# Kernel optimization log

Hardware: AMD Instinct MI355X
Metric: run time of the kernel (lower is better)

Reference implementation:

```python
import jax, jax.numpy as jnp
import numpy as np

N_NODES = 50000
N_EDGES = 1600000
IN_DIM = 128
HID = 128
N_GRAPHS = 64
N_CLASSES = 1


def _seg_sum(x, ids, n):
    return jax.ops.segment_sum(x, ids, num_segments=n)


def _gcn_layer(h, W, b, src, dst, src_isqrt, dst_isqrt):
    # DGL GraphConv, norm='both': D_dst^{-1/2} A D_src^{-1/2} (h W) + b
    hw = h @ W                                  # [N, out]
    msg = (hw * src_isqrt[:, None])[src]        # gather -> [E, out]
    agg = _seg_sum(msg, dst, h.shape[0])        # scatter-add -> [N, out]
    return agg * dst_isqrt[:, None] + b


def setup_inputs() -> dict:
    key = jax.random.key(0)
    ks = jax.random.split(key, 16)
    x = jax.random.normal(ks[0], (N_NODES, IN_DIM), dtype=jnp.float32)
    src = jax.random.randint(ks[1], (N_EDGES,), 0, N_NODES)
    dst = jax.random.randint(ks[2], (N_EDGES,), 0, N_NODES)
    graph_id = jnp.sort(jax.random.randint(ks[3], (N_NODES,), 0, N_GRAPHS))
    s = 1.0 / np.sqrt(HID)
    params = {
        'W1': jax.random.uniform(ks[4], (IN_DIM, HID), jnp.float32, -s, s),
        'b1': jnp.zeros((HID,), jnp.float32),
        'W2': jax.random.uniform(ks[5], (HID, HID), jnp.float32, -s, s),
        'b2': jnp.zeros((HID,), jnp.float32),
        'Wc1': jax.random.uniform(ks[6], (HID, HID // 2), jnp.float32, -s, s),
        'bc1': jnp.zeros((HID // 2,), jnp.float32),
        'Wc2': jax.random.uniform(ks[7], (HID // 2, HID // 4), jnp.float32, -s, s),
        'bc2': jnp.zeros((HID // 4,), jnp.float32),
        'Wc3': jax.random.uniform(ks[8], (HID // 4, HID // 8), jnp.float32, -s, s),
        'bc3': jnp.zeros((HID // 8,), jnp.float32),
        'Wc4': jax.random.uniform(ks[9], (HID // 8, N_CLASSES), jnp.float32, -s, s),
        'bc4': jnp.zeros((N_CLASSES,), jnp.float32),
    }
    return dict(x=x, src=src, dst=dst, graph_id=graph_id, num_graphs=N_GRAPHS, **params)


def reference(x, src, dst, graph_id, num_graphs, W1, b1, W2, b2,
              Wc1, bc1, Wc2, bc2, Wc3, bc3, Wc4, bc4):
    n = x.shape[0]
    ones = jnp.ones((src.shape[0],), x.dtype)
    out_deg = jnp.clip(_seg_sum(ones, src, n), 1.0)
    in_deg = jnp.clip(_seg_sum(ones, dst, n), 1.0)
    src_isqrt = jax.lax.rsqrt(out_deg)
    dst_isqrt = jax.lax.rsqrt(in_deg)

    h = jax.nn.relu(_gcn_layer(x, W1, b1, src, dst, src_isqrt, dst_isqrt))
    h = jax.nn.relu(_gcn_layer(h, W2, b2, src, dst, src_isqrt, dst_isqrt))

    # dgl.mean_nodes: per-graph mean of node features
    sums = _seg_sum(h, graph_id, num_graphs)                       # [G, HID]
    cnts = jnp.clip(_seg_sum(jnp.ones((n,), h.dtype), graph_id, num_graphs), 1.0)
    hg = sums / cnts[:, None]

    o = jax.nn.relu(hg @ Wc1 + bc1)
    o = jax.nn.relu(o @ Wc2 + bc2)
    o = jax.nn.relu(o @ Wc3 + bc3)
    return o @ Wc4 + bc4
```

## Files before the change

### kernel.cpp

```cpp
#include <hip/hip_runtime.h>
#include <hip/hip_fp16.h>

#define FDIM 128
#define NGRAPH 64
#define POOL_CHUNK 64
#define CBLK 256
#define OCHUNK 12800
#define OBLK 64

typedef _Float16 f16;
typedef f16 f16x8 __attribute__((ext_vector_type(8)));
typedef float f32x4 __attribute__((ext_vector_type(4)));
typedef float f32x2 __attribute__((ext_vector_type(2)));

__device__ __forceinline__ int lower_bound_i(const int* a, int n, int v) {
    int lo = 0, hi = n;
    while (lo < hi) { int m = (lo + hi) >> 1; if (a[m] < v) lo = m + 1; else hi = m; }
    return lo;
}

__global__ __launch_bounds__(256) void k_pre(
        const float* __restrict__ W1, f16* __restrict__ W1h, f16* __restrict__ W1l,
        const float* __restrict__ W2, f16* __restrict__ W2h, f16* __restrict__ W2l,
        float* __restrict__ hg, const int* __restrict__ dst, int* __restrict__ partial,
        int E, int NBIN, int CE4) {
    __shared__ int lds[4 * 257];
    const int t = threadIdx.x;
    int b = blockIdx.x;
    if (b < 128) {
        int i = b * 256 + t;
        if (i < NGRAPH * FDIM) hg[i] = 0.f;
        int j = i & 16383;
        int k = j >> 7, n = j & 127;
        const float* W = (i < 16384) ? W1 : W2;
        f16* Wh = (i < 16384) ? W1h : W2h;
        f16* Wl = (i < 16384) ? W1l : W2l;
        float v = W[j];
        f16 hi = (f16)v;
        Wh[n * FDIM + k] = hi;
        Wl[n * FDIM + k] = (f16)(v - (float)hi);
    } else {
        b -= 128;
        for (int i = t; i < 4 * 257; i += 256) lds[i] = 0;
        __syncthreads();
        const int wv = t >> 6;
        int* hh = &lds[wv * 257];
        const int s = b * CE4, e = min(E, s + CE4);
        for (int i = s + t * 4; i < e; i += 1024) {
            if (i + 4 <= e) {
                uint4 d4 = *(const uint4*)&dst[i];
                atomicAdd(&hh[d4.x >> 8], 1);
                atomicAdd(&hh[d4.y >> 8], 1);
                atomicAdd(&hh[d4.z >> 8], 1);
                atomicAdd(&hh[d4.w >> 8], 1);
            } else {
                for (int j = i; j < e; j++) atomicAdd(&hh[dst[j] >> 8], 1);
            }
        }
        __syncthreads();
        for (int i = t; i < NBIN; i += 256)
            partial[i * CBLK + b] = lds[i] + lds[257 + i] + lds[514 + i] + lds[771 + i];
    }
}

__global__ __launch_bounds__(256) void k_scan_oh(
        const int* __restrict__ partial, int* __restrict__ offs, int* __restrict__ bsum,
        int M, const int* __restrict__ src, int* __restrict__ out_part,
        int E, int N, int NBIN) {
    __shared__ int lds[OCHUNK];
    const int t = threadIdx.x;
    int b = blockIdx.x;
    if (b < NBIN) {
        int i = b * 256 + t;
        int v = (i < M) ? partial[i] : 0;
        lds[t] = v;
        __syncthreads();
        for (int off = 1; off < 256; off <<= 1) {
            int x = (t >= off) ? lds[t - off] : 0;
            __syncthreads();
            lds[t] += x;
            __syncthreads();
        }
        if (i < M) offs[i] = lds[t] - v;
        if (t == 255) bsum[b] = lds[t];
    } else {
        b -= NBIN;
        const int c = b / OBLK, sl = b % OBLK;
        for (int i = t; i < OCHUNK; i += 256) lds[i] = 0;
        __syncthreads();
        const int lo = c * OCHUNK;
        const int SE = (E + OBLK - 1) / OBLK;
        const int s = sl * SE, e = min(E, s + SE);
        for (int i = s + t * 4; i < e; i += 1024) {
            if (i + 4 <= e) {
                uint4 s4 = *(const uint4*)&src[i];
                int v0 = (int)s4.x - lo, v1 = (int)s4.y - lo;
                int v2 = (int)s4.z - lo, v3 = (int)s4.w - lo;
                if ((unsigned)v0 < (unsigned)OCHUNK) atomicAdd(&lds[v0], 1);
                if ((unsigned)v1 < (unsigned)OCHUNK) atomicAdd(&lds[v1], 1);
                if ((unsigned)v2 < (unsigned)OCHUNK) atomicAdd(&lds[v2], 1);
                if ((unsigned)v3 < (unsigned)OCHUNK) atomicAdd(&lds[v3], 1);
            } else {
                for (int j = i; j < e; j++) {
                    int v = src[j] - lo;
                    if ((unsigned)v < (unsigned)OCHUNK) atomicAdd(&lds[v], 1);
                }
            }
        }
        __syncthreads();
        const int hi = min(N - lo, OCHUNK);
        for (int i = t; i < hi; i += 256)
            out_part[(size_t)sl * N + lo + i] = lds[i];
    }
}

__global__ __launch_bounds__(256) void k_coarse_scatter(
        const int* __restrict__ src, const int* __restrict__ dst,
        const int* __restrict__ offs, const int* __restrict__ bsum,
        unsigned* __restrict__ coarse_buf, int E, int CE4, int NBIN) {
    __shared__ int cur[256], sb[256];
    const int t = threadIdx.x, b = blockIdx.x;
    int v = (t < NBIN) ? bsum[t] : 0;
    sb[t] = v;
    __syncthreads();
    for (int off = 1; off < 256; off <<= 1) {
        int x = (t >= off) ? sb[t - off] : 0;
        __syncthreads();
        sb[t] += x;
        __syncthreads();
    }
    if (t < NBIN) cur[t] = offs[t * CBLK + b] + (sb[t] - v);
    __syncthreads();
    const int s = b * CE4, e = min(E, s + CE4);
    for (int i = s + t * 4; i < e; i += 1024) {
        if (i + 4 <= e) {
            uint4 d4 = *(const uint4*)&dst[i];
            uint4 s4 = *(const uint4*)&src[i];
            int p0 = atomicAdd(&cur[d4.x >> 8], 1);
            int p1 = atomicAdd(&cur[d4.y >> 8], 1);
            int p2 = atomicAdd(&cur[d4.z >> 8], 1);
            int p3 = atomicAdd(&cur[d4.w >> 8], 1);
            coarse_buf[p0] = (d4.x << 16) | s4.x;
            coarse_buf[p1] = (d4.y << 16) | s4.y;
            coarse_buf[p2] = (d4.z << 16) | s4.z;
            coarse_buf[p3] = (d4.w << 16) | s4.w;
        } else {
            for (int j = i; j < e; j++) {
                unsigned d = (unsigned)dst[j];
                int p = atomicAdd(&cur[d >> 8], 1);
                coarse_buf[p] = (d << 16) | (unsigned)src[j];
            }
        }
    }
}

template<bool IN_F16>
__device__ __forceinline__ void gemm_body(
        f16* smem, float* sisql, int blk,
        const void* __restrict__ Xv, const f16* __restrict__ Wh,
        const f16* __restrict__ Wl, const int* __restrict__ out_part,
        float* __restrict__ sisq, unsigned char* __restrict__ out, int N) {
    const int t = threadIdx.x;
    const int w = t >> 6;
    const int lane = t & 63;
    const int base = blk * 128;

    if (t < 128) {
        int row = base + t;
        float sv = 1.f;
        if (row < N) {
            if (IN_F16) {
                sv = sisq[row];
            } else {
                int a = 0;
#pragma unroll
                for (int bb = 0; bb < OBLK; bb++) a += out_part[(size_t)bb * N + row];
                sv = rsqrtf((float)max(a, 1));
                sisq[row] = sv;
            }
        }
        sisql[t] = sv;
    }
    for (int i = t; i < 2048; i += 256) {
        int n = i >> 4, kc = (i & 15) * 8;
        *(uint4*)&smem[n * 136 + kc] = *(const uint4*)&Wh[n * FDIM + kc];
    }
    __syncthreads();

    const int mrow = lane & 15;
    const int kq = (lane >> 4) * 8;
    const int arow0 = min(base + w * 32 + mrow, N - 1);
    const int arow1 = min(base + w * 32 + 16 + mrow, N - 1);

    f16x8 a0[4], a1[4];
    if (IN_F16) {
        const f16* X = (const f16*)Xv;
#pragma unroll
        for (int kk = 0; kk < 4; kk++) {
            a0[kk] = *(const f16x8*)&X[(size_t)arow0 * FDIM + kk * 32 + kq];
            a1[kk] = *(const f16x8*)&X[(size_t)arow1 * FDIM + kk * 32 + kq];
        }
    } else {
        const float* X = (const float*)Xv;
#pragma unroll
        for (int kk = 0; kk < 4; kk++) {
            float4 u0 = *(const float4*)&X[(size_t)arow0 * FDIM + kk * 32 + kq];
            float4 u1 = *(const float4*)&X[(size_t)arow0 * FDIM + kk * 32 + kq + 4];
            float4 v0 = *(const float4*)&X[(size_t)arow1 * FDIM + kk * 32 + kq];
            float4 v1 = *(const float4*)&X[(size_t)arow1 * FDIM + kk * 32 + kq + 4];
            f16x8 av;
            av[0] = (f16)u0.x; av[1] = (f16)u0.y; av[2] = (f16)u0.z; av[3] = (f16)u0.w;
            av[4] = (f16)u1.x; av[5] = (f16)u1.y; av[6] = (f16)u1.z; av[7] = (f16)u1.w;
            a0[kk] = av;
            av[0] = (f16)v0.x; av[1] = (f16)v0.y; av[2] = (f16)v0.z; av[3] = (f16)v0.w;
            av[4] = (f16)v1.x; av[5] = (f16)v1.y; av[6] = (f16)v1.z; av[7] = (f16)v1.w;
            a1[kk] = av;
        }
    }

    f32x4 acc0[8], acc1[8];
#pragma unroll
    for (int nt = 0; nt < 8; nt++) {
        acc0[nt] = (f32x4){0.f, 0.f, 0.f, 0.f};
        acc1[nt] = (f32x4){0.f, 0.f, 0.f, 0.f};
    }

#pragma unroll
    for (int kk = 0; kk < 4; kk++) {
#pragma unroll
        for (int nt = 0; nt < 8; nt++) {
            f16x8 bh = *(const f16x8*)&smem[(nt * 16 + mrow) * 136 + kk * 32 + kq];
            f16x8 bl = *(const f16x8*)&Wl[(nt * 16 + mrow) * FDIM + kk * 32 + kq];
            acc0[nt] = __builtin_amdgcn_mfma_f32_16x16x32_f16(a0[kk], bh, acc0[nt], 0, 0, 0);
            acc1[nt] = __builtin_amdgcn_mfma_f32_16x16x32_f16(a1[kk], bh, acc1[nt], 0, 0, 0);
            acc0[nt] = __builtin_amdgcn_mfma_f32_16x16x32_f16(a0[kk], bl, acc0[nt], 0, 0, 0);
            acc1[nt] = __builtin_amdgcn_mfma_f32_16x16x32_f16(a1[kk], bl, acc1[nt], 0, 0, 0);
        }
    }

    const int r0 = (lane >> 4) * 4;
    float sv0[4], sv1[4];
#pragma unroll
    for (int j = 0; j < 4; j++) {
        sv0[j] = sisql[w * 32 + r0 + j];
        sv1[j] = sisql[w * 32 + 16 + r0 + j];
    }
    __syncthreads();
#pragma unroll
    for (int nt = 0; nt < 8; nt++) {
        int c = nt * 16 + mrow;
#pragma unroll
        for (int j = 0; j < 4; j++) {
            smem[(w * 32 + r0 + j) * 136 + c]      = (f16)(acc0[nt][j] * sv0[j]);
            smem[(w * 32 + 16 + r0 + j) * 136 + c] = (f16)(acc1[nt][j] * sv1[j]);
        }
    }
    __syncthreads();
    {
        int r = t >> 1, cb = (t & 1) * 64;
        int row = base + r;
        if (row < N) {
            unsigned char* dstp = out + (size_t)row * FDIM + cb;
#pragma unroll
            for (int g2 = 0; g2 < 4; g2++) {
                unsigned wv[4];
#pragma unroll
                for (int k2 = 0; k2 < 4; k2++) {
                    const f16* p = &smem[r * 136 + cb + g2 * 16 + k2 * 4];
                    int w0 = __builtin_amdgcn_cvt_pk_fp8_f32((float)p[0], (float)p[1], 0, false);
                    w0 = __builtin_amdgcn_cvt_pk_fp8_f32((float)p[2], (float)p[3], w0, true);
                    wv[k2] = (unsigned)w0;
                }
                uint4 u;
                u.x = wv[0]; u.y = wv[1]; u.z = wv[2]; u.w = wv[3];
                *(uint4*)&dstp[g2 * 16] = u;
            }
        }
    }
}

__global__ __launch_bounds__(256) void k_fine_gemm(
        const unsigned* __restrict__ coarse_buf, const int* __restrict__ bsum,
        int* __restrict__ csr_src, int* __restrict__ row_ptr, int N, int E, int NBIN,
        const float* __restrict__ x, const f16* __restrict__ Wh,
        const f16* __restrict__ Wl, const int* __restrict__ out_part,
        float* __restrict__ sisq, unsigned char* __restrict__ hws) {
    __shared__ __align__(16) f16 smem[128 * 136];
    __shared__ float sisql[128];
    const int t = threadIdx.x;
    const int g = blockIdx.x;
    if (g >= NBIN) {
        gemm_body<false>(smem, sisql, g - NBIN, x, Wh, Wl, out_part, sisq, hws, N);
        return;
    }
    int* h  = (int*)smem;
    int* sc = h + 256;
    int* cur = h + 512;
    int bv = (t < NBIN) ? bsum[t] : 0;
    sc[t] = bv;
    __syncthreads();
    for (int off = 1; off < 256; off <<= 1) {
        int xx = (t >= off) ? sc[t - off] : 0;
        __syncthreads();
        sc[t] += xx;
        __syncthreads();
    }
    __syncthreads();
    if (t == 0) { h[0] = sc[g] - bsum[g]; h[1] = sc[g]; }
    __syncthreads();
    const int s = h[0], e = h[1];
    __syncthreads();
    h[t] = 0;
    __syncthreads();
    for (int i = s + t; i < e; i += 256)
        atomicAdd(&h[(coarse_buf[i] >> 16) & 255], 1);
    __syncthreads();
    int v = h[t];
    sc[t] = v;
    __syncthreads();
    for (int off = 1; off < 256; off <<= 1) {
        int xx = (t >= off) ? sc[t - off] : 0;
        __syncthreads();
        sc[t] += xx;
        __syncthreads();
    }
    const int excl = sc[t] - v;
    const int node = g * 256 + t;
    if (node < N) row_ptr[node] = s + excl;
    if (node == N) row_ptr[N] = s + excl;
    cur[t] = s + excl;
    __syncthreads();
    for (int i = s + t; i < e; i += 256) {
        unsigned p = coarse_buf[i];
        int f = (p >> 16) & 255;
        int pos = atomicAdd(&cur[f], 1);
        csr_src[pos] = (int)(p & 0xFFFFu);
    }
    if (g == NBIN - 1 && t == 0 && (N & 255) == 0) row_ptr[N] = E;
}

__global__ __launch_bounds__(256) void k_gemm2(
        const f16* __restrict__ X, const f16* __restrict__ Wh,
        const f16* __restrict__ Wl, float* __restrict__ sisq,
        unsigned char* __restrict__ out, int N) {
    __shared__ __align__(16) f16 smem[128 * 136];
    __shared__ float sisql[128];
    gemm_body<true>(smem, sisql, blockIdx.x, X, Wh, Wl, nullptr, sisq, out, N);
}

__device__ __forceinline__ void accF8(float* acc, uint2 v) {
    f32x2 a0 = __builtin_amdgcn_cvt_pk_f32_fp8((int)v.x, false);
    f32x2 a1 = __builtin_amdgcn_cvt_pk_f32_fp8((int)v.x, true);
    f32x2 a2 = __builtin_amdgcn_cvt_pk_f32_fp8((int)v.y, false);
    f32x2 a3 = __builtin_amdgcn_cvt_pk_f32_fp8((int)v.y, true);
    acc[0] += a0.x; acc[1] += a0.y; acc[2] += a1.x; acc[3] += a1.y;
    acc[4] += a2.x; acc[5] += a2.y; acc[6] += a3.x; acc[7] += a3.y;
}

__global__ __launch_bounds__(256) void k_aggregate(
        const unsigned char* __restrict__ hws, const int* __restrict__ csr_src,
        const int* __restrict__ row_ptr,
        const float* __restrict__ bias, f16* __restrict__ out, int N) {
    const int t = threadIdx.x;
    const int node = blockIdx.x * 16 + (t >> 4);
    if (node >= N) return;
    const int fbase = (t & 15) * 8;

    const int s = row_ptr[node];
    const int e = row_ptr[node + 1];
    float acc[8];
#pragma unroll
    for (int j = 0; j < 8; j++) acc[j] = 0.f;

    int i = s;
    for (; i + 8 <= e; i += 8) {
        int u[8];
#pragma unroll
        for (int j = 0; j < 8; j++) u[j] = csr_src[i + j];
        uint2 v[8];
#pragma unroll
        for (int j = 0; j < 8; j++)
            v[j] = *(const uint2*)(hws + (size_t)u[j] * FDIM + fbase);
#pragma unroll
        for (int j = 0; j < 8; j++) accF8(acc, v[j]);
    }
    if (i + 4 <= e) {
        int u[4];
#pragma unroll
        for (int j = 0; j < 4; j++) u[j] = csr_src[i + j];
        uint2 v[4];
#pragma unroll
        for (int j = 0; j < 4; j++)
            v[j] = *(const uint2*)(hws + (size_t)u[j] * FDIM + fbase);
#pragma unroll
        for (int j = 0; j < 4; j++) accF8(acc, v[j]);
        i += 4;
    }
    for (; i < e; i++) {
        int u = csr_src[i];
        uint2 v = *(const uint2*)(hws + (size_t)u * FDIM + fbase);
        accF8(acc, v);
    }

    const float d = rsqrtf((float)max(e - s, 1));
    f16 res[8];
#pragma unroll
    for (int j = 0; j < 8; j++)
        res[j] = (f16)fmaxf(fmaf(acc[j], d, bias[fbase + j]), 0.f);
    *(uint4*)(out + (size_t)node * FDIM + fbase) = *(const uint4*)res;
}

__global__ void k_pool_sum(const f16* __restrict__ h, const int* __restrict__ gid,
                           float* __restrict__ hg, int N) {
    const int t = threadIdx.x;
    int s = blockIdx.x * POOL_CHUNK;
    int e = min(N, s + POOL_CHUNK);
    if (s >= e) return;
    int g = gid[s];
    float acc = 0.f;
    for (int n = s; n < e; n++) {
        int gn = gid[n];
        if (gn != g) {
            atomicAdd(&hg[g * FDIM + t], acc);
            acc = 0.f;
            g = gn;
        }
        acc += (float)h[(size_t)n * FDIM + t];
    }
    atomicAdd(&hg[g * FDIM + t], acc);
}

__global__ __launch_bounds__(256) void k_mlp(
        const float* __restrict__ hg, const int* __restrict__ gid, int N,
        const float* __restrict__ Wc1, const float* __restrict__ bc1,
        const float* __restrict__ Wc2, const float* __restrict__ bc2,
        const float* __restrict__ Wc3, const float* __restrict__ bc3,
        const float* __restrict__ Wc4, const float* __restrict__ bc4,
        float* __restrict__ out) {
    __shared__ float A[NGRAPH * 128];
    __shared__ float O1[NGRAPH * 64];
    __shared__ float O2[NGRAPH * 32];
    __shared__ float O3[NGRAPH * 16];
    __shared__ float inv_cnt[NGRAPH];
    const int t = threadIdx.x;

    if (t < NGRAPH) {
        int s = lower_bound_i(gid, N, t);
        int e = lower_bound_i(gid, N, t + 1);
        inv_cnt[t] = 1.f / fmaxf((float)(e - s), 1.f);
    }
    __syncthreads();

    for (int i = t; i < NGRAPH * 128; i += 256) A[i] = hg[i] * inv_cnt[i >> 7];
    __syncthreads();

    for (int i = t; i < NGRAPH * 64; i += 256) {
        int g = i >> 6, o = i & 63;
        float a = bc1[o];
        for (int k = 0; k < 128; k++) a = fmaf(A[g * 128 + k], Wc1[k * 64 + o], a);
        O1[i] = fmaxf(a, 0.f);
    }
    __syncthreads();

    for (int i = t; i < NGRAPH * 32; i += 256) {
        int g = i >> 5, o = i & 31;
        float a = bc2[o];
        for (int k = 0; k < 64; k++) a = fmaf(O1[g * 64 + k], Wc2[k * 32 + o], a);
        O2[i] = fmaxf(a, 0.f);
    }
    __syncthreads();

    for (int i = t; i < NGRAPH * 16; i += 256) {
        int g = i >> 4, o = i & 15;
        float a = bc3[o];
        for (int k = 0; k < 32; k++) a = fmaf(O2[g * 32 + k], Wc3[k * 16 + o], a);
        O3[i] = fmaxf(a, 0.f);
    }
    __syncthreads();

    if (t < NGRAPH) {
        float a = bc4[0];
        for (int k = 0; k < 16; k++) a = fmaf(O3[t * 16 + k], Wc4[k], a);
        out[t] = a;
    }
}

extern "C" void kernel_launch(void* const* d_in, const int* in_sizes, int n_in,
                              void* d_out, int out_size, void* d_ws, size_t ws_size,
                              hipStream_t stream) {
    const float* x   = (const float*)d_in[0];
    const int*   src = (const int*)d_in[1];
    const int*   dst = (const int*)d_in[2];
    const int*   gid = (const int*)d_in[3];
    const float* W1  = (const float*)d_in[5];
    const float* b1  = (const float*)d_in[6];
    const float* W2  = (const float*)d_in[7];
    const float* b2  = (const float*)d_in[8];
    const float* Wc1 = (const float*)d_in[9];
    const float* bc1 = (const float*)d_in[10];
    const float* Wc2 = (const float*)d_in[11];
    const float* bc2 = (const float*)d_in[12];
    const float* Wc3 = (const float*)d_in[13];
    const float* bc3 = (const float*)d_in[14];
    const float* Wc4 = (const float*)d_in[15];
    const float* bc4 = (const float*)d_in[16];
    float* out = (float*)d_out;

    const int N = in_sizes[0] / FDIM;
    const int E = in_sizes[1];

    const int NBIN = (N + 255) >> 8;
    const int M    = NBIN * CBLK;
    const int CE4  = (((E + CBLK - 1) / CBLK) + 3) & ~3;
    const int OC   = (N + OCHUNK - 1) / OCHUNK;

    char* w = (char*)d_ws;
    size_t off = 0;
    auto alloc = [&](size_t bytes) -> void* {
        void* p = w + off;
        off = (off + bytes + 255) & ~(size_t)255;
        return p;
    };
    unsigned char* hws = (unsigned char*)alloc((size_t)N * FDIM);
    f16*   h       = (f16*)   alloc((size_t)N * FDIM * 2);
    int*   csr_src = (int*)   alloc((size_t)E * 4);
    unsigned* coarse_buf = (unsigned*)alloc((size_t)E * 4);
    int*   out_part = (int*) alloc((size_t)OBLK * N * 4);
    int*   partial = (int*)   alloc((size_t)M * 4);
    int*   offs    = (int*)   alloc((size_t)M * 4);
    int*   row_ptr = (int*)   alloc((size_t)(N + 1) * 4);
    float* sisq    = (float*) alloc((size_t)N * 4);
    int*   bsum    = (int*)   alloc(256 * 4);
    float* hg      = (float*) alloc(NGRAPH * FDIM * 4);
    f16*   W1t     = (f16*)   alloc(FDIM * FDIM * 2);
    f16*   W1l     = (f16*)   alloc(FDIM * FDIM * 2);
    f16*   W2t     = (f16*)   alloc(FDIM * FDIM * 2);
    f16*   W2l     = (f16*)   alloc(FDIM * FDIM * 2);

    const int gT = (N + 127) / 128;
    const int gA = (N + 15) / 16;

    k_pre<<<128 + CBLK, 256, 0, stream>>>(
        W1, W1t, W1l, W2, W2t, W2l, hg, dst, partial, E, NBIN, CE4);
    k_scan_oh<<<NBIN + OC * OBLK, 256, 0, stream>>>(
        partial, offs, bsum, M, src, out_part, E, N, NBIN);
    k_coarse_scatter<<<CBLK, 256, 0, stream>>>(src, dst, offs, bsum, coarse_buf, E, CE4, NBIN);
    k_fine_gemm<<<NBIN + gT, 256, 0, stream>>>(
        coarse_buf, bsum, csr_src, row_ptr, N, E, NBIN,
        x, W1t, W1l, out_part, sisq, hws);
    k_aggregate<<<gA, 256, 0, stream>>>(hws, csr_src, row_ptr, b1, h, N);
    k_gemm2<<<gT, 256, 0, stream>>>(h, W2t, W2l, sisq, hws, N);
    k_aggregate<<<gA, 256, 0, stream>>>(hws, csr_src, row_ptr, b2, h, N);
    const int gP = (N + POOL_CHUNK - 1) / POOL_CHUNK;
    k_pool_sum<<<gP, 128, 0, stream>>>(h, gid, hg, N);
    k_mlp<<<1, 256, 0, stream>>>(hg, gid, N, Wc1, bc1, Wc2, bc2, Wc3, bc3, Wc4, bc4, out);
}
```

Measured before the change: 284.7 us.

## Fold prefix scan into coarse scatter and merge out-degree histogram into pre kernel

```diff
diff --git a/kernel.cpp b/kernel.cpp
--- a/kernel.cpp
+++ b/kernel.cpp
@@ -23,8 +23,9 @@
         const float* __restrict__ W1, f16* __restrict__ W1h, f16* __restrict__ W1l,
         const float* __restrict__ W2, f16* __restrict__ W2h, f16* __restrict__ W2l,
         float* __restrict__ hg, const int* __restrict__ dst, int* __restrict__ partial,
-        int E, int NBIN, int CE4) {
-    __shared__ int lds[4 * 257];
+        const int* __restrict__ src, int* __restrict__ out_part,
+        int E, int N, int NBIN, int CE4) {
+    __shared__ int lds[OCHUNK];
     const int t = threadIdx.x;
     int b = blockIdx.x;
     if (b < 128) {
@@ -39,7 +40,7 @@
         f16 hi = (f16)v;
         Wh[n * FDIM + k] = hi;
         Wl[n * FDIM + k] = (f16)(v - (float)hi);
-    } else {
+    } else if (b < 128 + CBLK) {
         b -= 128;
         for (int i = t; i < 4 * 257; i += 256) lds[i] = 0;
         __syncthreads();
@@ -60,31 +61,8 @@
         __syncthreads();
         for (int i = t; i < NBIN; i += 256)
             partial[i * CBLK + b] = lds[i] + lds[257 + i] + lds[514 + i] + lds[771 + i];
-    }
-}
-
-__global__ __launch_bounds__(256) void k_scan_oh(
-        const int* __restrict__ partial, int* __restrict__ offs, int* __restrict__ bsum,
-        int M, const int* __restrict__ src, int* __restrict__ out_part,
-        int E, int N, int NBIN) {
-    __shared__ int lds[OCHUNK];
-    const int t = threadIdx.x;
-    int b = blockIdx.x;
-    if (b < NBIN) {
-        int i = b * 256 + t;
-        int v = (i < M) ? partial[i] : 0;
-        lds[t] = v;
-        __syncthreads();
-        for (int off = 1; off < 256; off <<= 1) {
-            int x = (t >= off) ? lds[t - off] : 0;
-            __syncthreads();
-            lds[t] += x;
-            __syncthreads();
-        }
-        if (i < M) offs[i] = lds[t] - v;
-        if (t == 255) bsum[b] = lds[t];
     } else {
-        b -= NBIN;
+        b -= (128 + CBLK);
         const int c = b / OBLK, sl = b % OBLK;
         for (int i = t; i < OCHUNK; i += 256) lds[i] = 0;
         __syncthreads();
@@ -116,12 +94,24 @@
 
 __global__ __launch_bounds__(256) void k_coarse_scatter(
         const int* __restrict__ src, const int* __restrict__ dst,
-        const int* __restrict__ offs, const int* __restrict__ bsum,
-        unsigned* __restrict__ coarse_buf, int E, int CE4, int NBIN) {
+        const int* __restrict__ partial, unsigned* __restrict__ coarse_buf,
+        int* __restrict__ bsum, int E, int CE4, int NBIN) {
     __shared__ int cur[256], sb[256];
     const int t = threadIdx.x, b = blockIdx.x;
-    int v = (t < NBIN) ? bsum[t] : 0;
-    sb[t] = v;
+    int tot = 0, psum = 0;
+    if (t < NBIN) {
+        const int* row = &partial[t * CBLK];
+        for (int j = 0; j < CBLK; j += 4) {
+            int4 v = *(const int4*)&row[j];
+            tot += v.x + v.y + v.z + v.w;
+            psum += ((j     < b) ? v.x : 0);
+            psum += ((j + 1 < b) ? v.y : 0);
+            psum += ((j + 2 < b) ? v.z : 0);
+            psum += ((j + 3 < b) ? v.w : 0);
+        }
+        if (b == 0) bsum[t] = tot;
+    }
+    sb[t] = (t < NBIN) ? tot : 0;
     __syncthreads();
     for (int off = 1; off < 256; off <<= 1) {
         int x = (t >= off) ? sb[t - off] : 0;
@@ -129,7 +119,7 @@
         sb[t] += x;
         __syncthreads();
     }
-    if (t < NBIN) cur[t] = offs[t * CBLK + b] + (sb[t] - v);
+    if (t < NBIN) cur[t] = (sb[t] - tot) + psum;
     __syncthreads();
     const int s = b * CE4, e = min(E, s + CE4);
     for (int i = s + t * 4; i < e; i += 1024) {
@@ -527,7 +517,6 @@
     unsigned* coarse_buf = (unsigned*)alloc((size_t)E * 4);
     int*   out_part = (int*) alloc((size_t)OBLK * N * 4);
     int*   partial = (int*)   alloc((size_t)M * 4);
-    int*   offs    = (int*)   alloc((size_t)M * 4);
     int*   row_ptr = (int*)   alloc((size_t)(N + 1) * 4);
     float* sisq    = (float*) alloc((size_t)N * 4);
     int*   bsum    = (int*)   alloc(256 * 4);
@@ -540,11 +529,9 @@
     const int gT = (N + 127) / 128;
     const int gA = (N + 15) / 16;
 
-    k_pre<<<128 + CBLK, 256, 0, stream>>>(
-        W1, W1t, W1l, W2, W2t, W2l, hg, dst, partial, E, NBIN, CE4);
-    k_scan_oh<<<NBIN + OC * OBLK, 256, 0, stream>>>(
-        partial, offs, bsum, M, src, out_part, E, N, NBIN);
-    k_coarse_scatter<<<CBLK, 256, 0, stream>>>(src, dst, offs, bsum, coarse_buf, E, CE4, NBIN);
+    k_pre<<<128 + CBLK + OC * OBLK, 256, 0, stream>>>(
+        W1, W1t, W1l, W2, W2t, W2l, hg, dst, partial, src, out_part, E, N, NBIN, CE4);
+    k_coarse_scatter<<<CBLK, 256, 0, stream>>>(src, dst, partial, coarse_buf, bsum, E, CE4, NBIN);
     k_fine_gemm<<<NBIN + gT, 256, 0, stream>>>(
         coarse_buf, bsum, csr_src, row_ptr, N, E, NBIN,
         x, W1t, W1l, out_part, sisq, hws);
```

Result: no change. 289.7 us (+1.7%).
